# Kernel optimization log

Measured on AMD Instinct MI355X. Metric: run time of the kernel, lower is better.

Reference implementation:

```python
import jax, jax.numpy as jnp
import numpy as np

B, N, F_IN, H, K, ITERS = 8, 2048, 64, 64, 50, 2


def topk_mask(S, k):
    # sparse_topk: keep the k largest entries of each row, zeros elsewhere
    vals, idx = jax.lax.top_k(S, k)                # [B, N, k]
    b = jnp.arange(S.shape[0])[:, None, None]
    r = jnp.arange(S.shape[1])[None, :, None]
    return jnp.zeros_like(S).at[b, r, idx].set(vals)


def setup_inputs() -> dict:
    key = jax.random.key(0)
    ks = jax.random.split(key, 8)

    def w(k, shape, fan_in):
        return jax.random.normal(k, shape, jnp.float32) / np.sqrt(fan_in)

    z = lambda d: jnp.zeros((d,), jnp.float32)
    return {
        "x": jax.random.normal(ks[0], (B, N, F_IN), jnp.float32),
        "emb_w0": w(ks[1], (F_IN, H), F_IN), "emb_b0": z(H),
        "emb_w1": w(ks[2], (H, H), H),       "emb_b1": z(H),
        "mp0_wm": w(ks[3], (H, H), H),       "mp0_bm": z(H),
        "mp0_wu": w(ks[4], (2 * H, H), 2 * H), "mp0_bu": z(H),
        "mp1_wm": w(ks[5], (H, H), H),       "mp1_bm": z(H),
        "mp1_wu": w(ks[6], (2 * H, H), 2 * H), "mp1_bu": z(H),
    }


def reference(x, emb_w0, emb_b0, emb_w1, emb_b1,
              mp0_wm, mp0_bm, mp0_wu, mp0_bu,
              mp1_wm, mp1_bm, mp1_wu, mp1_bu):
    # node embedding: 2-layer MLP (emb_init=2)
    h = jax.nn.relu(x @ emb_w0 + emb_b0)
    h = jax.nn.relu(h @ emb_w1 + emb_b1)

    mp_params = [(mp0_wm, mp0_bm, mp0_wu, mp0_bu),
                 (mp1_wm, mp1_bm, mp1_wu, mp1_bu)]
    for wm, bm, wu, bu in mp_params:
        # dense similarity, then per-row top-k sparsification (sparse_topk)
        S = jnp.einsum('bnd,bmd->bnm', h, h)       # [B, N, N]
        A = topk_mask(S, K)                        # sparse adjacency (as masked dense)
        msg = jax.nn.relu(h @ wm + bm)             # message fn
        agg = jnp.einsum('bnm,bmd->bnd', A, msg)   # sparse mm aggregation
        h = jax.nn.relu(jnp.concatenate([h, agg], axis=-1) @ wu + bu)

    S = jnp.einsum('bnd,bmd->bnm', h, h)
    return topk_mask(S, K)                         # dense top-k adjacency [B, N, N]
```

## Files before the change

kernel.cpp:

```cpp
#include <hip/hip_runtime.h>

#define N_NODES 2048
#define KSEL 50

typedef float v2f __attribute__((ext_vector_type(2)));

__device__ __forceinline__ unsigned ford(float f) {
  unsigned b = __float_as_uint(f);
  return b ^ ((b & 0x80000000u) ? 0xFFFFFFFFu : 0x80000000u);
}
__device__ __forceinline__ float funord(unsigned u) {
  unsigned b = (u & 0x80000000u) ? (u ^ 0x80000000u) : ~u;
  return __uint_as_float(b);
}

__device__ __forceinline__ int hidx1(unsigned b) {
  return (int)(((b & 63u) << 2) | (b >> 6));
}

__device__ __forceinline__ void mlp_layer(float acc[16], const float* xs,
                                          const float* Ws, const float* bs,
                                          int r, int cg) {
  const float4* Ws4 = (const float4*)Ws;
#pragma unroll
  for (int i = 0; i < 16; ++i) acc[i] = bs[cg * 16 + i];
#pragma unroll 8
  for (int k = 0; k < 64; ++k) {
    float xv = xs[k * 65 + r];
    float4 w0 = Ws4[k * 16 + cg * 4 + 0];
    float4 w1 = Ws4[k * 16 + cg * 4 + 1];
    float4 w2 = Ws4[k * 16 + cg * 4 + 2];
    float4 w3 = Ws4[k * 16 + cg * 4 + 3];
    acc[0]  += xv * w0.x; acc[1]  += xv * w0.y; acc[2]  += xv * w0.z; acc[3]  += xv * w0.w;
    acc[4]  += xv * w1.x; acc[5]  += xv * w1.y; acc[6]  += xv * w1.z; acc[7]  += xv * w1.w;
    acc[8]  += xv * w2.x; acc[9]  += xv * w2.y; acc[10] += xv * w2.z; acc[11] += xv * w2.w;
    acc[12] += xv * w3.x; acc[13] += xv * w3.y; acc[14] += xv * w3.z; acc[15] += xv * w3.w;
  }
#pragma unroll
  for (int i = 0; i < 16; ++i) acc[i] = fmaxf(acc[i], 0.f);
}

__global__ __launch_bounds__(256) void emb3_kernel(
    const float* __restrict__ x,
    const float* __restrict__ ew0, const float* __restrict__ eb0,
    const float* __restrict__ ew1, const float* __restrict__ eb1,
    const float* __restrict__ wmm, const float* __restrict__ bmm,
    float* __restrict__ outA, float* __restrict__ outAT, float* __restrict__ outM)
{
  const int tid = threadIdx.x;
  const int r = tid & 63, cg = tid >> 6;
  const size_t rowbase = (size_t)blockIdx.x * 64;
  __shared__ float xs[64 * 65];
  __shared__ float Ws[64 * 64];
  __shared__ float bs[64];
  float acc[16];

#pragma unroll
  for (int i = 0; i < 16; ++i) {
    int idx = tid + 256 * i;
    xs[(idx & 63) * 65 + (idx >> 6)] = x[rowbase * 64 + idx];
    Ws[idx] = ew0[idx];
  }
  if (tid < 64) bs[tid] = eb0[tid];
  __syncthreads();
  mlp_layer(acc, xs, Ws, bs, r, cg);
  __syncthreads();
#pragma unroll
  for (int i = 0; i < 16; ++i) {
    xs[(cg * 16 + i) * 65 + r] = acc[i];
    Ws[tid + 256 * i] = ew1[tid + 256 * i];
  }
  if (tid < 64) bs[tid] = eb1[tid];
  __syncthreads();
  mlp_layer(acc, xs, Ws, bs, r, cg);
  {
    float4* o4 = (float4*)(outA + (rowbase + r) * 64 + cg * 16);
#pragma unroll
    for (int q = 0; q < 4; ++q)
      o4[q] = make_float4(acc[q*4+0], acc[q*4+1], acc[q*4+2], acc[q*4+3]);
  }
  __syncthreads();
#pragma unroll
  for (int i = 0; i < 16; ++i) {
    xs[(cg * 16 + i) * 65 + r] = acc[i];
    Ws[tid + 256 * i] = wmm[tid + 256 * i];
  }
  if (tid < 64) bs[tid] = bmm[tid];
  __syncthreads();
  {
    const size_t bb = rowbase >> 11;
    const int nbase = (int)(rowbase & 2047);
    const int c = tid >> 2, seg = tid & 3;
    float* oT = outAT + bb * 64 * N_NODES + (size_t)c * N_NODES + nbase + seg * 16;
#pragma unroll
    for (int q = 0; q < 4; ++q)
      ((float4*)oT)[q] = make_float4(xs[c*65+seg*16+q*4+0], xs[c*65+seg*16+q*4+1],
                                     xs[c*65+seg*16+q*4+2], xs[c*65+seg*16+q*4+3]);
  }
  mlp_layer(acc, xs, Ws, bs, r, cg);
  {
    float4* o4 = (float4*)(outM + (rowbase + r) * 64 + cg * 16);
#pragma unroll
    for (int q = 0; q < 4; ++q)
      o4[q] = make_float4(acc[q*4+0], acc[q*4+1], acc[q*4+2], acc[q*4+3]);
  }
}

__global__ __launch_bounds__(256) void linrelu_kernel(
    const float* __restrict__ in, const float* __restrict__ W,
    const float* __restrict__ bias, float* __restrict__ out)
{
  const int tid = threadIdx.x;
  const int r = tid & 63, cg = tid >> 6;
  const size_t rowbase = (size_t)blockIdx.x * 64;
  __shared__ float xs[64 * 65];
  __shared__ float Ws[64 * 64];
  __shared__ float bs[64];
  float acc[16];
#pragma unroll
  for (int i = 0; i < 16; ++i) {
    int idx = tid + 256 * i;
    xs[(idx & 63) * 65 + (idx >> 6)] = in[rowbase * 64 + idx];
    Ws[idx] = W[idx];
  }
  if (tid < 64) bs[tid] = bias[tid];
  __syncthreads();
  mlp_layer(acc, xs, Ws, bs, r, cg);
  float4* o4 = (float4*)(out + (rowbase + r) * 64 + cg * 16);
#pragma unroll
  for (int q = 0; q < 4; ++q)
    o4[q] = make_float4(acc[q*4+0], acc[q*4+1], acc[q*4+2], acc[q*4+3]);
}

template <bool FINAL>
__global__ __launch_bounds__(512, 4) void mp_kernel(
    const float* __restrict__ h, const float* __restrict__ hT,
    const float* __restrict__ msg,
    const float* __restrict__ wu, const float* __restrict__ bu,
    float* __restrict__ outp, float* __restrict__ outT)
{
  const int tid = threadIdx.x;
  const int lane = tid & 63;
  const int w64 = tid >> 6;
  const int bid = blockIdx.x;
  const int b = bid & 7;
  const int n0 = (bid >> 3) * 8;

  __shared__ unsigned Sbuf[8 * N_NODES];
  __shared__ unsigned hist[8][256];
  __shared__ float hrL[8 * 64];
  __shared__ unsigned LwMin[8][8], LwMax[8][8];
  __shared__ int   seli[8][52];
  __shared__ float selv[8][52];
  __shared__ int   eqlist[8][64];

  const float* hb  = h  + (size_t)b * N_NODES * 64;
  const float* hTb = hT + (size_t)b * 64 * N_NODES;
  const float* colp = hTb + 4 * tid;

  float4 pf[4];
#pragma unroll
  for (int i = 0; i < 4; ++i) pf[i] = *(const float4*)(colp + (size_t)i * 2048);

  if (!FINAL) hrL[tid] = hb[(size_t)n0 * 64 + tid];
  for (int i = tid; i < 8 * 256; i += 512) (&hist[0][0])[i] = 0;

  v2f acc2[16];
#pragma unroll
  for (int i = 0; i < 16; ++i) { acc2[i][0] = 0.f; acc2[i][1] = 0.f; }

  const float* hrow = hb + (size_t)n0 * 64;
  for (int k4 = 0; k4 < 16; ++k4) {
    float4 a[8];
#pragma unroll
    for (int r = 0; r < 8; ++r)
      a[r] = *(const float4*)(hrow + r * 64 + k4 * 4);
#pragma unroll
    for (int kk = 0; kk < 4; ++kk) {
      const int k = k4 * 4 + kk;
      float4 cu = pf[kk];
      if (k + 4 < 64) pf[kk] = *(const float4*)(colp + (size_t)(k + 4) * 2048);
      v2f c00 = {cu.x, cu.y}, c01 = {cu.z, cu.w};
#pragma unroll
      for (int r = 0; r < 8; ++r) {
        const float ar = ((const float*)&a[r])[kk];
        v2f as = {ar, ar};
        acc2[r*2+0] = __builtin_elementwise_fma(as, c00, acc2[r*2+0]);
        acc2[r*2+1] = __builtin_elementwise_fma(as, c01, acc2[r*2+1]);
      }
    }
  }

#pragma unroll
  for (int r = 0; r < 8; ++r) {
    uint4 w;
    w.x = ford(acc2[r*2+0][0]); w.y = ford(acc2[r*2+0][1]);
    w.z = ford(acc2[r*2+1][0]); w.w = ford(acc2[r*2+1][1]);
    *(uint4*)&Sbuf[r * N_NODES + 4 * tid] = w;
    unsigned m1 = w.x > w.y ? w.x : w.y, m2 = w.z > w.w ? w.z : w.w;
    unsigned lm = m1 > m2 ? m1 : m2;
    unsigned mn = lm, mx = lm;
#pragma unroll
    for (int off = 32; off >= 1; off >>= 1) {
      unsigned o1 = (unsigned)__shfl_xor((int)mn, off, 64);
      unsigned o2 = (unsigned)__shfl_xor((int)mx, off, 64);
      mn = mn < o1 ? mn : o1;
      mx = mx > o2 ? mx : o2;
    }
    if (lane == 0) { LwMin[w64][r] = mn; LwMax[w64][r] = mx; }
  }
  __syncthreads();

  const int rw = w64;
  const unsigned* Srow = &Sbuf[rw * N_NODES];
  unsigned Lv, Tv;
  {
    unsigned lmn = (lane < 8) ? LwMin[lane][rw] : 0u;
    unsigned lmx = (lane < 8) ? LwMax[lane][rw] : 0u;
#pragma unroll
    for (int off = 4; off >= 1; off >>= 1) {
      unsigned o1 = (unsigned)__shfl_xor((int)lmn, off, 8);
      unsigned o2 = (unsigned)__shfl_xor((int)lmx, off, 8);
      lmn = lmn > o1 ? lmn : o1;
      lmx = lmx > o2 ? lmx : o2;
    }
    Lv = (unsigned)__shfl((int)lmn, 0, 64);
    unsigned Mv = (unsigned)__shfl((int)lmx, 0, 64);

    if (Lv == Mv) {
      Tv = Mv;
    } else {
      int sh = 24 - 8 * (__builtin_clz(Lv ^ Mv) >> 3);
      unsigned pv = (unsigned)(((unsigned long long)Lv) >> (sh + 8));
      unsigned Kc = KSEL;
      int mode = 0;
      unsigned* hrw = hist[rw];
      for (int it = 0; it < 5 && mode != 2; ++it) {
        const int s2 = sh + 8;
        const unsigned lo = (s2 >= 32) ? 0u : (pv << s2);
        const unsigned hi = (s2 >= 32) ? 0xFFFFFFFFu : (lo | ((1u << s2) - 1u));
        const unsigned lo2 = lo > Lv ? lo : Lv;
        if (mode == 0) {
#pragma unroll
          for (int i = 0; i < 8; ++i) {
            uint4 q = *(const uint4*)&Srow[i * 256 + 4 * lane];
            unsigned vv[4] = {q.x, q.y, q.z, q.w};
#pragma unroll
            for (int e = 0; e < 4; ++e) {
              unsigned v = vv[e];
              if (v >= lo2 && v <= hi)
                atomicAdd(&hrw[hidx1((v >> sh) & 255u)], 1u);
            }
          }
          uint4 q = *(const uint4*)&hrw[lane * 4];
          *(uint4*)&hrw[lane * 4] = make_uint4(0, 0, 0, 0);
          unsigned c0 = q.x, c1 = q.y, c2 = q.z, c3 = q.w;
          unsigned s0 = c0, s1 = c1, s2s = c2, s3 = c3;
#pragma unroll
          for (int off = 1; off < 64; off <<= 1) {
            unsigned t0=__shfl_down((int)s0,off,64), t1=__shfl_down((int)s1,off,64);
            unsigned t2=__shfl_down((int)s2s,off,64), t3=__shfl_down((int)s3,off,64);
            if (lane + off < 64) { s0+=t0; s1+=t1; s2s+=t2; s3+=t3; }
          }
          unsigned T1=(unsigned)__shfl((int)s1,0,64);
          unsigned T2=(unsigned)__shfl((int)s2s,0,64);
          unsigned T3=(unsigned)__shfl((int)s3,0,64);
          unsigned cA[4] = {c0, c1, c2, c3};
          unsigned AA[4] = {s0 - c0 + T1 + T2 + T3, s1 - c1 + T2 + T3,
                            s2s - c2 + T3,          s3 - c3};
          int fg = -1;
#pragma unroll
          for (int g = 0; g < 4; ++g)
            if (AA[g] < Kc && Kc <= AA[g] + cA[g]) fg = g;
          unsigned long long mk = __ballot(fg >= 0);
          int src = __ffsll(mk) - 1;
          unsigned bin = 0, nKc = 0, cnt = 0;
          if (fg >= 0) {
            bin = (unsigned)(fg * 64 + lane);
            nKc = Kc - AA[fg];
            cnt = cA[fg];
          }
          bin = (unsigned)__shfl((int)bin, src, 64);
          nKc = (unsigned)__shfl((int)nKc, src, 64);
          cnt = (unsigned)__shfl((int)cnt, src, 64);
          pv = (pv << 8) | bin;
          Kc = nKc;
          sh -= 8;
          if (sh < 0)        { Tv = pv; mode = 2; }
          else if (cnt == 1) mode = 1;
        } else {
          unsigned found = 0; bool has = false;
#pragma unroll
          for (int i = 0; i < 8; ++i) {
            uint4 q = *(const uint4*)&Srow[i * 256 + 4 * lane];
            unsigned vv[4] = {q.x, q.y, q.z, q.w};
#pragma unroll
            for (int e = 0; e < 4; ++e) {
              unsigned v = vv[e];
              if (v >= lo2 && v <= hi) { found = v; has = true; }
            }
          }
          unsigned long long mk = __ballot(has);
          int src = __ffsll(mk) - 1;
          Tv = (unsigned)__shfl((int)found, src, 64);
          mode = 2;
        }
      }
    }
  }

  unsigned vals[32];
  int cgt = 0, ceq = 0;
#pragma unroll
  for (int i = 0; i < 8; ++i) {
    uint4 q = *(const uint4*)&Srow[i * 256 + 4 * lane];
    vals[i*4+0] = q.x; vals[i*4+1] = q.y; vals[i*4+2] = q.z; vals[i*4+3] = q.w;
#pragma unroll
    for (int e = 0; e < 4; ++e) {
      cgt += (vals[i*4+e] > Tv);
      ceq += (vals[i*4+e] == Tv);
    }
  }
  int sg = cgt, se = ceq;
#pragma unroll
  for (int off = 1; off < 64; off <<= 1) {
    int t0 = __shfl_up(sg, off, 64), t1 = __shfl_up(se, off, 64);
    if (lane >= off) { sg += t0; se += t1; }
  }
  const int gW = __shfl(sg, 63, 64);
  const int eTot = __shfl(se, 63, 64);
  int gb = sg - cgt, eb = se - ceq;
#pragma unroll
  for (int i = 0; i < 8; ++i) {
#pragma unroll
    for (int e = 0; e < 4; ++e) {
      unsigned v = vals[i*4+e];
      int m = i * 256 + 4 * lane + e;
      if (v > Tv) { seli[rw][gb] = m; selv[rw][gb] = funord(v); ++gb; }
      else if (v == Tv) { if (eb < 64) eqlist[rw][eb] = m; ++eb; }
    }
  }
  const int eW = eTot < 64 ? eTot : 64;

  const int needW = KSEL - gW;
  {
    const float Tf = funord(Tv);
    int myi = (lane < eW) ? eqlist[rw][lane] : 0x7FFFFFFF;
    for (int t = 0; t < needW; ++t) {
      int mn = myi;
#pragma unroll
      for (int off = 32; off >= 1; off >>= 1) {
        int o = __shfl_xor(mn, off, 64);
        mn = mn < o ? mn : o;
      }
      if (mn == 0x7FFFFFFF) break;
      if (myi == mn) {
        seli[rw][gW + t] = mn; selv[rw][gW + t] = Tf;
        myi = 0x7FFFFFFF;
      }
    }
  }

  if constexpr (FINAL) {
    float* ob = outp + ((size_t)b * N_NODES + n0 + rw) * N_NODES;
#pragma unroll
    for (int i = 0; i < 8; ++i) {
      float4 w; float* wf = (float*)&w;
#pragma unroll
      for (int e = 0; e < 4; ++e) {
        const unsigned v = vals[i*4+e];
        const int m = i * 256 + 4 * lane + e;
        bool keep = v > Tv;
        if (v == Tv) {
          for (int t = 0; t < needW; ++t)
            if (seli[rw][gW + t] == m) { keep = true; break; }
        }
        wf[e] = keep ? funord(v) : 0.f;
      }
      *(float4*)(ob + i * 256 + 4 * lane) = w;
    }
  } else {
    float* aggbR = (float*)&Sbuf[rw * N_NODES + 1024];
    {
      const float* msgb = msg + (size_t)b * N_NODES * 64;
      float a = 0.f;
      for (int i = 0; i < KSEL; ++i) {
        int mi = seli[rw][i];
        float vvv = selv[rw][i];
        a += vvv * msgb[(size_t)mi * 64 + lane];
      }
      aggbR[lane] = a;
    }
    float s = bu[lane];
#pragma unroll 8
    for (int jj = 0; jj < 64; ++jj)
      s += hrL[rw * 64 + jj] * wu[jj * 64 + lane];
#pragma unroll 8
    for (int jj = 0; jj < 64; ++jj)
      s += aggbR[jj] * wu[(64 + jj) * 64 + lane];
    s = fmaxf(s, 0.f);
    outp[((size_t)b * N_NODES + n0 + rw) * 64 + lane] = s;
    __syncthreads();
    float* otF = (float*)Sbuf;
    otF[lane * 9 + rw] = s;
    __syncthreads();
    {
      int f = tid >> 3, rr = tid & 7;
      outT[(size_t)b * 64 * N_NODES + (size_t)f * N_NODES + n0 + rr] = otF[f * 9 + rr];
    }
  }
}

extern "C" void kernel_launch(void* const* d_in, const int* in_sizes, int n_in,
                              void* d_out, int out_size, void* d_ws, size_t ws_size,
                              hipStream_t stream)
{
  (void)in_sizes; (void)n_in; (void)out_size; (void)ws_size;
  const float* x   = (const float*)d_in[0];
  const float* ew0 = (const float*)d_in[1];
  const float* eb0 = (const float*)d_in[2];
  const float* ew1 = (const float*)d_in[3];
  const float* eb1 = (const float*)d_in[4];
  const float* w0m = (const float*)d_in[5];
  const float* b0m = (const float*)d_in[6];
  const float* w0u = (const float*)d_in[7];
  const float* b0u = (const float*)d_in[8];
  const float* w1m = (const float*)d_in[9];
  const float* b1m = (const float*)d_in[10];
  const float* w1u = (const float*)d_in[11];
  const float* b1u = (const float*)d_in[12];
  float* out = (float*)d_out;
  float* ws = (float*)d_ws;

  const size_t BUF = (size_t)8 * N_NODES * 64;
  float* A   = ws;
  float* AT  = ws + 1 * BUF;
  float* Bf  = ws + 2 * BUF;
  float* BfT = ws + 3 * BUF;
  float* C   = ws + 4 * BUF;

  emb3_kernel<<<256, 256, 0, stream>>>(x, ew0, eb0, ew1, eb1, w0m, b0m, A, AT, C);

  mp_kernel<false><<<2048, 512, 0, stream>>>(A, AT, C, w0u, b0u, Bf, BfT);

  linrelu_kernel<<<256, 256, 0, stream>>>(Bf, w1m, b1m, C);

  mp_kernel<false><<<2048, 512, 0, stream>>>(Bf, BfT, C, w1u, b1u, A, AT);

  mp_kernel<true><<<2048, 512, 0, stream>>>(A, AT, nullptr, nullptr, nullptr, out, nullptr);
}
```

Measured before the change: 609.5 us.

## Use 4-row blocks with two column halves per thread; simplify final top-k write

Each block now handles 4 rows with 256 threads, and each thread computes two column chunks (offsets 0 and 1024) per row instead of one. This halves shared-memory use per block and doubles the number of blocks, which could raise occupancy. The FINAL path now writes rows in one pass: values above the threshold are stored directly, then the tie entries equal to the threshold are scattered afterwards, replacing the per-element search over the selected list. The trade-off is that each column load is now reused across fewer rows per block, and the tie list shrinks from 64 to 56 entries.

After: 546.7 us. -10.3%, faster.

```diff
diff --git a/kernel.cpp b/kernel.cpp
--- a/kernel.cpp
+++ b/kernel.cpp
@@ -2,6 +2,7 @@
 
 #define N_NODES 2048
 #define KSEL 50
+#define ROWS 4
 
 typedef float v2f __attribute__((ext_vector_type(2)));
 
@@ -133,7 +134,7 @@
 }
 
 template <bool FINAL>
-__global__ __launch_bounds__(512, 4) void mp_kernel(
+__global__ __launch_bounds__(256, 4) void mp_kernel(
     const float* __restrict__ h, const float* __restrict__ hT,
     const float* __restrict__ msg,
     const float* __restrict__ wu, const float* __restrict__ bu,
@@ -144,26 +145,29 @@
   const int w64 = tid >> 6;
   const int bid = blockIdx.x;
   const int b = bid & 7;
-  const int n0 = (bid >> 3) * 8;
-
-  __shared__ unsigned Sbuf[8 * N_NODES];
-  __shared__ unsigned hist[8][256];
-  __shared__ float hrL[8 * 64];
-  __shared__ unsigned LwMin[8][8], LwMax[8][8];
-  __shared__ int   seli[8][52];
-  __shared__ float selv[8][52];
-  __shared__ int   eqlist[8][64];
+  const int n0 = (bid >> 3) * ROWS;
+
+  __shared__ unsigned Sbuf[ROWS * N_NODES];
+  __shared__ unsigned hist[ROWS][256];
+  __shared__ float    hrL[ROWS * 64];
+  __shared__ unsigned LwMin[ROWS][ROWS], LwMax[ROWS][ROWS];
+  __shared__ int   seli[ROWS][52];
+  __shared__ float selv[ROWS][52];
+  __shared__ int   eqlist[ROWS][56];
 
   const float* hb  = h  + (size_t)b * N_NODES * 64;
   const float* hTb = hT + (size_t)b * 64 * N_NODES;
   const float* colp = hTb + 4 * tid;
 
-  float4 pf[4];
-#pragma unroll
-  for (int i = 0; i < 4; ++i) pf[i] = *(const float4*)(colp + (size_t)i * 2048);
+  float4 pfA[4], pfB[4];
+#pragma unroll
+  for (int i = 0; i < 4; ++i) {
+    pfA[i] = *(const float4*)(colp + (size_t)i * 2048);
+    pfB[i] = *(const float4*)(colp + (size_t)i * 2048 + 1024);
+  }
 
   if (!FINAL) hrL[tid] = hb[(size_t)n0 * 64 + tid];
-  for (int i = tid; i < 8 * 256; i += 512) (&hist[0][0])[i] = 0;
+  for (int i = tid; i < ROWS * 256; i += 256) (&hist[0][0])[i] = 0;
 
   v2f acc2[16];
 #pragma unroll
@@ -171,34 +175,45 @@
 
   const float* hrow = hb + (size_t)n0 * 64;
   for (int k4 = 0; k4 < 16; ++k4) {
-    float4 a[8];
-#pragma unroll
-    for (int r = 0; r < 8; ++r)
+    float4 a[ROWS];
+#pragma unroll
+    for (int r = 0; r < ROWS; ++r)
       a[r] = *(const float4*)(hrow + r * 64 + k4 * 4);
 #pragma unroll
     for (int kk = 0; kk < 4; ++kk) {
       const int k = k4 * 4 + kk;
-      float4 cu = pf[kk];
-      if (k + 4 < 64) pf[kk] = *(const float4*)(colp + (size_t)(k + 4) * 2048);
-      v2f c00 = {cu.x, cu.y}, c01 = {cu.z, cu.w};
-#pragma unroll
-      for (int r = 0; r < 8; ++r) {
+      float4 cA = pfA[kk], cB = pfB[kk];
+      if (k + 4 < 64) {
+        pfA[kk] = *(const float4*)(colp + (size_t)(k + 4) * 2048);
+        pfB[kk] = *(const float4*)(colp + (size_t)(k + 4) * 2048 + 1024);
+      }
+      v2f cA0 = {cA.x, cA.y}, cA1 = {cA.z, cA.w};
+      v2f cB0 = {cB.x, cB.y}, cB1 = {cB.z, cB.w};
+#pragma unroll
+      for (int r = 0; r < ROWS; ++r) {
         const float ar = ((const float*)&a[r])[kk];
         v2f as = {ar, ar};
-        acc2[r*2+0] = __builtin_elementwise_fma(as, c00, acc2[r*2+0]);
-        acc2[r*2+1] = __builtin_elementwise_fma(as, c01, acc2[r*2+1]);
-      }
-    }
-  }
-
-#pragma unroll
-  for (int r = 0; r < 8; ++r) {
-    uint4 w;
-    w.x = ford(acc2[r*2+0][0]); w.y = ford(acc2[r*2+0][1]);
-    w.z = ford(acc2[r*2+1][0]); w.w = ford(acc2[r*2+1][1]);
-    *(uint4*)&Sbuf[r * N_NODES + 4 * tid] = w;
-    unsigned m1 = w.x > w.y ? w.x : w.y, m2 = w.z > w.w ? w.z : w.w;
-    unsigned lm = m1 > m2 ? m1 : m2;
+        acc2[r*4+0] = __builtin_elementwise_fma(as, cA0, acc2[r*4+0]);
+        acc2[r*4+1] = __builtin_elementwise_fma(as, cA1, acc2[r*4+1]);
+        acc2[r*4+2] = __builtin_elementwise_fma(as, cB0, acc2[r*4+2]);
+        acc2[r*4+3] = __builtin_elementwise_fma(as, cB1, acc2[r*4+3]);
+      }
+    }
+  }
+
+#pragma unroll
+  for (int r = 0; r < ROWS; ++r) {
+    uint4 wA, wB;
+    wA.x = ford(acc2[r*4+0][0]); wA.y = ford(acc2[r*4+0][1]);
+    wA.z = ford(acc2[r*4+1][0]); wA.w = ford(acc2[r*4+1][1]);
+    wB.x = ford(acc2[r*4+2][0]); wB.y = ford(acc2[r*4+2][1]);
+    wB.z = ford(acc2[r*4+3][0]); wB.w = ford(acc2[r*4+3][1]);
+    *(uint4*)&Sbuf[r * N_NODES + 4 * tid] = wA;
+    *(uint4*)&Sbuf[r * N_NODES + 1024 + 4 * tid] = wB;
+    unsigned mA1 = wA.x > wA.y ? wA.x : wA.y, mA2 = wA.z > wA.w ? wA.z : wA.w;
+    unsigned mB1 = wB.x > wB.y ? wB.x : wB.y, mB2 = wB.z > wB.w ? wB.z : wB.w;
+    unsigned mA = mA1 > mA2 ? mA1 : mA2, mB = mB1 > mB2 ? mB1 : mB2;
+    unsigned lm = mA > mB ? mA : mB;
     unsigned mn = lm, mx = lm;
 #pragma unroll
     for (int off = 32; off >= 1; off >>= 1) {
@@ -215,12 +230,12 @@
   const unsigned* Srow = &Sbuf[rw * N_NODES];
   unsigned Lv, Tv;
   {
-    unsigned lmn = (lane < 8) ? LwMin[lane][rw] : 0u;
-    unsigned lmx = (lane < 8) ? LwMax[lane][rw] : 0u;
-#pragma unroll
-    for (int off = 4; off >= 1; off >>= 1) {
-      unsigned o1 = (unsigned)__shfl_xor((int)lmn, off, 8);
-      unsigned o2 = (unsigned)__shfl_xor((int)lmx, off, 8);
+    unsigned lmn = (lane < ROWS) ? LwMin[lane][rw] : 0u;
+    unsigned lmx = (lane < ROWS) ? LwMax[lane][rw] : 0u;
+#pragma unroll
+    for (int off = 2; off >= 1; off >>= 1) {
+      unsigned o1 = (unsigned)__shfl_xor((int)lmn, off, 4);
+      unsigned o2 = (unsigned)__shfl_xor((int)lmx, off, 4);
       lmn = lmn > o1 ? lmn : o1;
       lmx = lmx > o2 ? lmx : o2;
     }
@@ -265,20 +280,20 @@
           unsigned T1=(unsigned)__shfl((int)s1,0,64);
           unsigned T2=(unsigned)__shfl((int)s2s,0,64);
           unsigned T3=(unsigned)__shfl((int)s3,0,64);
-          unsigned cA[4] = {c0, c1, c2, c3};
+          unsigned cA4[4] = {c0, c1, c2, c3};
           unsigned AA[4] = {s0 - c0 + T1 + T2 + T3, s1 - c1 + T2 + T3,
                             s2s - c2 + T3,          s3 - c3};
           int fg = -1;
 #pragma unroll
           for (int g = 0; g < 4; ++g)
-            if (AA[g] < Kc && Kc <= AA[g] + cA[g]) fg = g;
+            if (AA[g] < Kc && Kc <= AA[g] + cA4[g]) fg = g;
           unsigned long long mk = __ballot(fg >= 0);
           int src = __ffsll(mk) - 1;
           unsigned bin = 0, nKc = 0, cnt = 0;
           if (fg >= 0) {
             bin = (unsigned)(fg * 64 + lane);
             nKc = Kc - AA[fg];
-            cnt = cA[fg];
+            cnt = cA4[fg];
           }
           bin = (unsigned)__shfl((int)bin, src, 64);
           nKc = (unsigned)__shfl((int)nKc, src, 64);
@@ -330,21 +345,37 @@
   const int gW = __shfl(sg, 63, 64);
   const int eTot = __shfl(se, 63, 64);
   int gb = sg - cgt, eb = se - ceq;
-#pragma unroll
-  for (int i = 0; i < 8; ++i) {
-#pragma unroll
-    for (int e = 0; e < 4; ++e) {
-      unsigned v = vals[i*4+e];
-      int m = i * 256 + 4 * lane + e;
-      if (v > Tv) { seli[rw][gb] = m; selv[rw][gb] = funord(v); ++gb; }
-      else if (v == Tv) { if (eb < 64) eqlist[rw][eb] = m; ++eb; }
-    }
-  }
-  const int eW = eTot < 64 ? eTot : 64;
+
+  float* ob = FINAL ? (outp + ((size_t)b * N_NODES + n0 + rw) * N_NODES) : nullptr;
+  if constexpr (FINAL) {
+#pragma unroll
+    for (int i = 0; i < 8; ++i) {
+      float4 w; float* wf = (float*)&w;
+#pragma unroll
+      for (int e = 0; e < 4; ++e) {
+        unsigned v = vals[i*4+e];
+        wf[e] = (v > Tv) ? funord(v) : 0.f;
+        if (v == Tv) { if (eb < 56) eqlist[rw][eb] = i * 256 + 4 * lane + e; ++eb; }
+      }
+      *(float4*)(ob + i * 256 + 4 * lane) = w;
+    }
+  } else {
+#pragma unroll
+    for (int i = 0; i < 8; ++i) {
+#pragma unroll
+      for (int e = 0; e < 4; ++e) {
+        unsigned v = vals[i*4+e];
+        int m = i * 256 + 4 * lane + e;
+        if (v > Tv) { seli[rw][gb] = m; selv[rw][gb] = funord(v); ++gb; }
+        else if (v == Tv) { if (eb < 56) eqlist[rw][eb] = m; ++eb; }
+      }
+    }
+  }
+  const int eW = eTot < 56 ? eTot : 56;
 
   const int needW = KSEL - gW;
+  const float Tf = funord(Tv);
   {
-    const float Tf = funord(Tv);
     int myi = (lane < eW) ? eqlist[rw][lane] : 0x7FFFFFFF;
     for (int t = 0; t < needW; ++t) {
       int mn = myi;
@@ -355,30 +386,15 @@
       }
       if (mn == 0x7FFFFFFF) break;
       if (myi == mn) {
-        seli[rw][gW + t] = mn; selv[rw][gW + t] = Tf;
+        if (!FINAL) { seli[rw][gW + t] = mn; selv[rw][gW + t] = Tf; }
+        else eqlist[rw][t] = mn;
         myi = 0x7FFFFFFF;
       }
     }
   }
 
   if constexpr (FINAL) {
-    float* ob = outp + ((size_t)b * N_NODES + n0 + rw) * N_NODES;
-#pragma unroll
-    for (int i = 0; i < 8; ++i) {
-      float4 w; float* wf = (float*)&w;
-#pragma unroll
-      for (int e = 0; e < 4; ++e) {
-        const unsigned v = vals[i*4+e];
-        const int m = i * 256 + 4 * lane + e;
-        bool keep = v > Tv;
-        if (v == Tv) {
-          for (int t = 0; t < needW; ++t)
-            if (seli[rw][gW + t] == m) { keep = true; break; }
-        }
-        wf[e] = keep ? funord(v) : 0.f;
-      }
-      *(float4*)(ob + i * 256 + 4 * lane) = w;
-    }
+    if (lane < needW) ob[eqlist[rw][lane]] = Tf;
   } else {
     float* aggbR = (float*)&Sbuf[rw * N_NODES + 1024];
     {
@@ -405,7 +421,7 @@
     otF[lane * 9 + rw] = s;
     __syncthreads();
     {
-      int f = tid >> 3, rr = tid & 7;
+      int f = tid >> 2, rr = tid & 3;
       outT[(size_t)b * 64 * N_NODES + (size_t)f * N_NODES + n0 + rr] = otF[f * 9 + rr];
     }
   }
@@ -439,13 +455,15 @@
   float* BfT = ws + 3 * BUF;
   float* C   = ws + 4 * BUF;
 
+  const int NBLK = 8 * (N_NODES / ROWS);
+
   emb3_kernel<<<256, 256, 0, stream>>>(x, ew0, eb0, ew1, eb1, w0m, b0m, A, AT, C);
 
-  mp_kernel<false><<<2048, 512, 0, stream>>>(A, AT, C, w0u, b0u, Bf, BfT);
+  mp_kernel<false><<<NBLK, 256, 0, stream>>>(A, AT, C, w0u, b0u, Bf, BfT);
 
   linrelu_kernel<<<256, 256, 0, stream>>>(Bf, w1m, b1m, C);
 
-  mp_kernel<false><<<2048, 512, 0, stream>>>(Bf, BfT, C, w1u, b1u, A, AT);
-
-  mp_kernel<true><<<2048, 512, 0, stream>>>(A, AT, nullptr, nullptr, nullptr, out, nullptr);
-}
+  mp_kernel<false><<<NBLK, 256, 0, stream>>>(Bf, BfT, C, w1u, b1u, A, AT);
+
+  mp_kernel<true><<<NBLK, 256, 0, stream>>>(A, AT, nullptr, nullptr, nullptr, out, nullptr);
+}
```
